# Kernel optimization log

Hardware: AMD Instinct MI355X
Metric: run time of the kernel (lower is better)

## Reference

```python
import jax, jax.numpy as jnp
import numpy as np

N_NODES = 50000
N_EDGES = 800000
D = 64


def setup_inputs() -> dict:
    key = jax.random.key(0)
    ks = jax.random.split(key, 8)
    x = jax.random.normal(ks[0], (N_NODES, D), dtype=jnp.float32)
    edge_index = jax.random.randint(ks[1], (2, N_EDGES), 0, N_NODES, dtype=jnp.int64)
    # GCNConv params (PyG: Linear without bias inside lin, bias added after aggregation)
    def glorot(k, fan_in, fan_out):
        lim = (6.0 / (fan_in + fan_out)) ** 0.5
        return jax.random.uniform(k, (fan_in, fan_out), jnp.float32, -lim, lim)
    W1 = glorot(ks[2], D, D); b1 = jnp.zeros((D,), jnp.float32)
    W2 = glorot(ks[3], D, D); b2 = jnp.zeros((D,), jnp.float32)
    W3 = glorot(ks[4], D, D); b3 = jnp.zeros((D,), jnp.float32)
    return {"x": x, "edge_index": edge_index,
            "W1": W1, "b1": b1, "W2": W2, "b2": b2, "W3": W3, "b3": b3}


def _gcn_norm(edge_index, n_nodes, dtype):
    # Add self-loops, compute symmetric normalization D^-1/2 (A+I) D^-1/2 (PyG GCNConv default).
    loop = jnp.arange(n_nodes, dtype=edge_index.dtype)
    src = jnp.concatenate([edge_index[0], loop])  # message source j
    dst = jnp.concatenate([edge_index[1], loop])  # aggregation target i
    deg = jax.ops.segment_sum(jnp.ones_like(dst, dtype=dtype), dst, num_segments=n_nodes)
    dinv = jnp.where(deg > 0, jax.lax.rsqrt(deg), 0.0)
    norm = dinv[src] * dinv[dst]  # [E + N]
    return src, dst, norm


def _gcn_conv(x, src, dst, norm, W, b, n_nodes):
    h = x @ W                              # [N, D_out]
    msg = h[src] * norm[:, None]           # gather + scale, [E+N, D_out]
    out = jax.ops.segment_sum(msg, dst, num_segments=n_nodes)  # scatter-add
    return out + b


def reference(x, edge_index, W1, b1, W2, b2, W3, b3):
    n = x.shape[0]
    src, dst, norm = _gcn_norm(edge_index, n, x.dtype)
    # layer 0: conv -> relu -> residual
    h = _gcn_conv(x, src, dst, norm, W1, b1, n)
    h = jax.nn.relu(h) + x
    # layer 1: conv -> relu -> residual
    r = h
    h = _gcn_conv(h, src, dst, norm, W2, b2, n)
    h = jax.nn.relu(h) + r
    # layer 2 (final): conv only
    h = _gcn_conv(h, src, dst, norm, W3, b3, n)
    return h
```

## Files before the change

### kernel.cpp

```cpp
#include <hip/hip_runtime.h>
#include <hip/hip_bf16.h>


#define CAP 64
#define EDGE_CHUNK 1024

typedef __attribute__((ext_vector_type(8))) short bf16x8;
typedef __attribute__((ext_vector_type(4))) float f32x4;

__device__ inline unsigned pack_bf16(float a, float b) {
    union { float f; unsigned i; } ua, ub;
    ua.f = a; ub.f = b;
    unsigned x = (ua.i + 0x7fffu + ((ua.i >> 16) & 1u)) >> 16;
    unsigned y = (ub.i + 0x7fffu + ((ub.i >> 16) & 1u)) >> 16;
    return x | (y << 16);
}
__device__ inline unsigned short to_bf16(float a) {
    union { float f; unsigned i; } u; u.f = a;
    return (unsigned short)((u.i + 0x7fffu + ((u.i >> 16) & 1u)) >> 16);
}
__device__ inline void acc_bf16x2(unsigned u, float& a, float& b) {
    union { unsigned i; float f; } lo, hi;
    lo.i = u << 16;
    hi.i = u & 0xffff0000u;
    a += lo.f; b += hi.f;
}

__device__ inline void gather_plane(const unsigned short* __restrict__ gp,
                                    const int* __restrict__ lst, int deg, int off,
                                    float& a0, float& a1, float& a2, float& a3,
                                    float& a4, float& a5, float& a6, float& a7) {
    int nfull = deg >> 3;
    int4 ja, jb;
    if (nfull > 0) { ja = *(const int4*)&lst[0]; jb = *(const int4*)&lst[4]; }
    for (int b = 0; b < nfull; b++) {
        int4 na = ja, nb = jb;
        if (b + 1 < nfull) {
            na = *(const int4*)&lst[(b + 1) * 8];
            nb = *(const int4*)&lst[(b + 1) * 8 + 4];
        }
        uint4 w0 = *(const uint4*)&gp[(size_t)ja.x * 32 + off];
        uint4 w1 = *(const uint4*)&gp[(size_t)ja.y * 32 + off];
        uint4 w2 = *(const uint4*)&gp[(size_t)ja.z * 32 + off];
        uint4 w3 = *(const uint4*)&gp[(size_t)ja.w * 32 + off];
        uint4 w4 = *(const uint4*)&gp[(size_t)jb.x * 32 + off];
        uint4 w5 = *(const uint4*)&gp[(size_t)jb.y * 32 + off];
        uint4 w6 = *(const uint4*)&gp[(size_t)jb.z * 32 + off];
        uint4 w7 = *(const uint4*)&gp[(size_t)jb.w * 32 + off];
        acc_bf16x2(w0.x, a0, a1); acc_bf16x2(w0.y, a2, a3);
        acc_bf16x2(w0.z, a4, a5); acc_bf16x2(w0.w, a6, a7);
        acc_bf16x2(w1.x, a0, a1); acc_bf16x2(w1.y, a2, a3);
        acc_bf16x2(w1.z, a4, a5); acc_bf16x2(w1.w, a6, a7);
        acc_bf16x2(w2.x, a0, a1); acc_bf16x2(w2.y, a2, a3);
        acc_bf16x2(w2.z, a4, a5); acc_bf16x2(w2.w, a6, a7);
        acc_bf16x2(w3.x, a0, a1); acc_bf16x2(w3.y, a2, a3);
        acc_bf16x2(w3.z, a4, a5); acc_bf16x2(w3.w, a6, a7);
        acc_bf16x2(w4.x, a0, a1); acc_bf16x2(w4.y, a2, a3);
        acc_bf16x2(w4.z, a4, a5); acc_bf16x2(w4.w, a6, a7);
        acc_bf16x2(w5.x, a0, a1); acc_bf16x2(w5.y, a2, a3);
        acc_bf16x2(w5.z, a4, a5); acc_bf16x2(w5.w, a6, a7);
        acc_bf16x2(w6.x, a0, a1); acc_bf16x2(w6.y, a2, a3);
        acc_bf16x2(w6.z, a4, a5); acc_bf16x2(w6.w, a6, a7);
        acc_bf16x2(w7.x, a0, a1); acc_bf16x2(w7.y, a2, a3);
        acc_bf16x2(w7.z, a4, a5); acc_bf16x2(w7.w, a6, a7);
        ja = na; jb = nb;
    }
    int k = nfull * 8;
    if (k + 4 <= deg) {
        int4 j4 = *(const int4*)&lst[k];
        uint4 w0 = *(const uint4*)&gp[(size_t)j4.x * 32 + off];
        uint4 w1 = *(const uint4*)&gp[(size_t)j4.y * 32 + off];
        uint4 w2 = *(const uint4*)&gp[(size_t)j4.z * 32 + off];
        uint4 w3 = *(const uint4*)&gp[(size_t)j4.w * 32 + off];
        acc_bf16x2(w0.x, a0, a1); acc_bf16x2(w0.y, a2, a3);
        acc_bf16x2(w0.z, a4, a5); acc_bf16x2(w0.w, a6, a7);
        acc_bf16x2(w1.x, a0, a1); acc_bf16x2(w1.y, a2, a3);
        acc_bf16x2(w1.z, a4, a5); acc_bf16x2(w1.w, a6, a7);
        acc_bf16x2(w2.x, a0, a1); acc_bf16x2(w2.y, a2, a3);
        acc_bf16x2(w2.z, a4, a5); acc_bf16x2(w2.w, a6, a7);
        acc_bf16x2(w3.x, a0, a1); acc_bf16x2(w3.y, a2, a3);
        acc_bf16x2(w3.z, a4, a5); acc_bf16x2(w3.w, a6, a7);
        k += 4;
    }
    for (; k < deg; k++) {
        uint4 v = *(const uint4*)&gp[(size_t)lst[k] * 32 + off];
        acc_bf16x2(v.x, a0, a1); acc_bf16x2(v.y, a2, a3);
        acc_bf16x2(v.z, a4, a5); acc_bf16x2(v.w, a6, a7);
    }
}

__global__ void fill_kernel(const int* __restrict__ src, const int* __restrict__ dst,
                            int* __restrict__ cnt, int* __restrict__ adj,
                            int E, int npc) {
    int cls = blockIdx.x & 7;
    int base = (blockIdx.x >> 3) * EDGE_CHUNK;
    int end = min(base + EDGE_CHUNK, E);
    int lo = cls * npc, hi = lo + npc;
    for (int e = base + threadIdx.x; e < end; e += blockDim.x) {
        int d = dst[e];
        if (d >= lo && d < hi) {
            int p = atomicAdd(&cnt[d], 1);
            adj[(size_t)d * CAP + p] = src[e];
        }
    }
}

__device__ inline void stage_W(const float* __restrict__ W, unsigned short* Wb, int t) {
#pragma unroll
    for (int e0 = 0; e0 < 2; e0++) {
        int e = t + e0 * 256;
        int sc = e >> 6;
        int l  = e & 63;
        int s = sc >> 2, c = sc & 3;
        int nn = c * 16 + (l & 15);
        int kb = s * 32 + (l >> 4) * 8;
        const float* wp = &W[(size_t)kb * 64 + nn];
        unsigned q0 = pack_bf16(wp[0 * 64], wp[1 * 64]);
        unsigned q1 = pack_bf16(wp[2 * 64], wp[3 * 64]);
        unsigned q2 = pack_bf16(wp[4 * 64], wp[5 * 64]);
        unsigned q3 = pack_bf16(wp[6 * 64], wp[7 * 64]);
        *(uint4*)&Wb[e * 8] = make_uint4(q0, q1, q2, q3);
    }
}

__global__ __launch_bounds__(256, 4) void gemm_kernel(const float* __restrict__ in,
                                                      const float* __restrict__ W,
                                                      const int* __restrict__ cnt,
                                                      unsigned short* __restrict__ gLo,
                                                      unsigned short* __restrict__ gHi,
                                                      int n) {
    __shared__ unsigned short Wb[512 * 8];
    int t = threadIdx.x;
    stage_W(W, Wb, t);

    int wv = t >> 6;
    int lane = t & 63;
    int quad = lane >> 4;
    int m16 = lane & 15;

    int rowA = blockIdx.x * 64 + wv * 16 + m16;
    union { bf16x8 v; uint4 u; } a0, a1;
    {
        float4 f0 = make_float4(0, 0, 0, 0), f1 = f0, f2 = f0, f3 = f0;
        if (rowA < n) {
            const float* rp = &in[(size_t)rowA * 64];
            f0 = *(const float4*)&rp[quad * 8];
            f1 = *(const float4*)&rp[quad * 8 + 4];
            f2 = *(const float4*)&rp[32 + quad * 8];
            f3 = *(const float4*)&rp[32 + quad * 8 + 4];
        }
        a0.u = make_uint4(pack_bf16(f0.x, f0.y), pack_bf16(f0.z, f0.w),
                          pack_bf16(f1.x, f1.y), pack_bf16(f1.z, f1.w));
        a1.u = make_uint4(pack_bf16(f2.x, f2.y), pack_bf16(f2.z, f2.w),
                          pack_bf16(f3.x, f3.y), pack_bf16(f3.z, f3.w));
    }
    __syncthreads();

    f32x4 acc[4];
#pragma unroll
    for (int c = 0; c < 4; c++) {
        bf16x8 b0 = *(const bf16x8*)&Wb[((size_t)(0 * 4 + c) * 64 + lane) * 8];
        bf16x8 b1 = *(const bf16x8*)&Wb[((size_t)(1 * 4 + c) * 64 + lane) * 8];
        f32x4 z = {0.f, 0.f, 0.f, 0.f};
        z = __builtin_amdgcn_mfma_f32_16x16x32_bf16(a0.v, b0, z, 0, 0, 0);
        z = __builtin_amdgcn_mfma_f32_16x16x32_bf16(a1.v, b1, z, 0, 0, 0);
        acc[c] = z;
    }

    int lrow = wv * 16 + quad * 4;
    float dv[4];
#pragma unroll
    for (int r = 0; r < 4; r++) {
        int row = blockIdx.x * 64 + lrow + r;
        dv[r] = (row < n) ? rsqrtf((float)(cnt[row] + 1)) : 0.f;
    }
    __syncthreads();
    unsigned short* Ofrag = Wb;
#pragma unroll
    for (int c = 0; c < 4; c++) {
#pragma unroll
        for (int r = 0; r < 4; r++)
            Ofrag[(size_t)(lrow + r) * 64 + c * 16 + m16] = to_bf16(acc[c][r] * dv[r]);
    }
    __syncthreads();
#pragma unroll
    for (int it = 0; it < 2; it++) {
        int unit = t + it * 256;
        int row = unit >> 3, chv = unit & 7;
        int grow = blockIdx.x * 64 + row;
        if (grow < n) {
            unsigned short* op = (chv < 4) ? gLo : gHi;
            *(uint4*)&op[(size_t)grow * 32 + (chv & 3) * 8] =
                *(const uint4*)&Ofrag[(size_t)row * 64 + chv * 8];
        }
    }
}

template <int WRITE_H, int RES_BF16>
__global__ __launch_bounds__(256, 4) void aggemm_kernel(
        const unsigned short* __restrict__ gLo,
        const unsigned short* __restrict__ gHi,
        const int* __restrict__ cnt,
        const int* __restrict__ adj,
        const float* __restrict__ bias,
        const void* __restrict__ res_p,
        const float* __restrict__ W,
        unsigned short* __restrict__ h_out,
        unsigned short* __restrict__ goLo,
        unsigned short* __restrict__ goHi,
        int n) {
    __shared__ unsigned short Wb[512 * 8];
    __shared__ unsigned short Afrag[2048];
    __shared__ float dsh[32];
    int t = threadIdx.x;

    int r  = t >> 3;
    int lg = t & 7;
    const int c8 = lg * 8;
    const int po = (lg & 3) * 8;
    int i = blockIdx.x * 32 + r;
    bool valid = i < n;
    int deg = valid ? cnt[i] : 0;
    const int* lst = adj + (size_t)i * CAP;
    const unsigned short* mp = (lg < 4) ? gLo : gHi;

    float a0 = 0.f, a1 = 0.f, a2 = 0.f, a3 = 0.f;
    float a4 = 0.f, a5 = 0.f, a6 = 0.f, a7 = 0.f;
    float r0 = 0.f, r1 = 0.f, r2 = 0.f, r3 = 0.f;
    float r4 = 0.f, r5 = 0.f, r6 = 0.f, r7 = 0.f;
    if (valid) {
        {
            uint4 v = *(const uint4*)&mp[(size_t)i * 32 + po];
            acc_bf16x2(v.x, a0, a1); acc_bf16x2(v.y, a2, a3);
            acc_bf16x2(v.z, a4, a5); acc_bf16x2(v.w, a6, a7);
        }
        if (RES_BF16) {
            const unsigned short* rp = (const unsigned short*)res_p;
            uint4 rv = *(const uint4*)&rp[(size_t)i * 64 + c8];
            acc_bf16x2(rv.x, r0, r1); acc_bf16x2(rv.y, r2, r3);
            acc_bf16x2(rv.z, r4, r5); acc_bf16x2(rv.w, r6, r7);
        } else {
            const float* rp = (const float*)res_p;
            float4 q0 = *(const float4*)&rp[(size_t)i * 64 + c8];
            float4 q1 = *(const float4*)&rp[(size_t)i * 64 + c8 + 4];
            r0 = q0.x; r1 = q0.y; r2 = q0.z; r3 = q0.w;
            r4 = q1.x; r5 = q1.y; r6 = q1.z; r7 = q1.w;
        }
    }
    if (lg < 4)
        gather_plane(mp, lst, deg, po, a0, a1, a2, a3, a4, a5, a6, a7);
    __syncthreads();
    if (lg >= 4)
        gather_plane(mp, lst, deg, po, a0, a1, a2, a3, a4, a5, a6, a7);

    float dvv = 0.f;
    float v0 = 0.f, v1 = 0.f, v2 = 0.f, v3 = 0.f;
    float v4 = 0.f, v5 = 0.f, v6 = 0.f, v7 = 0.f;
    if (valid) {
        dvv = rsqrtf((float)(deg + 1));
        float4 b0 = *(const float4*)&bias[c8];
        float4 b1 = *(const float4*)&bias[c8 + 4];
        v0 = fmaxf(dvv * a0 + b0.x, 0.f) + r0;
        v1 = fmaxf(dvv * a1 + b0.y, 0.f) + r1;
        v2 = fmaxf(dvv * a2 + b0.z, 0.f) + r2;
        v3 = fmaxf(dvv * a3 + b0.w, 0.f) + r3;
        v4 = fmaxf(dvv * a4 + b1.x, 0.f) + r4;
        v5 = fmaxf(dvv * a5 + b1.y, 0.f) + r5;
        v6 = fmaxf(dvv * a6 + b1.z, 0.f) + r6;
        v7 = fmaxf(dvv * a7 + b1.w, 0.f) + r7;
    }
    uint4 pk;
    pk.x = pack_bf16(v0, v1);
    pk.y = pack_bf16(v2, v3);
    pk.z = pack_bf16(v4, v5);
    pk.w = pack_bf16(v6, v7);
    if (WRITE_H && valid)
        *(uint4*)&h_out[(size_t)i * 64 + c8] = pk;
    stage_W(W, Wb, t);
    {
        int sA = r >> 4, mA = r & 15;
        *(uint4*)&Afrag[((size_t)(sA * 8 + lg) * 16 + mA) * 8] = pk;
        if (lg == 0) dsh[r] = dvv;
    }
    __syncthreads();

    int wv = t >> 6;
    int lane = t & 63;
    int quad = lane >> 4;
    int m16 = lane & 15;
    int sB = wv & 1;
    int ch = wv >> 1;
    bf16x8 af0 = *(const bf16x8*)&Afrag[((size_t)(sB * 8 + quad) * 16 + m16) * 8];
    bf16x8 af1 = *(const bf16x8*)&Afrag[((size_t)(sB * 8 + 4 + quad) * 16 + m16) * 8];
    int lrow = sB * 16 + quad * 4;
    float dv2[4];
#pragma unroll
    for (int rr = 0; rr < 4; rr++)
        dv2[rr] = dsh[lrow + rr];
    __syncthreads();
    f32x4 acc[2];
#pragma unroll
    for (int c2 = 0; c2 < 2; c2++) {
        int c = ch * 2 + c2;
        bf16x8 b0 = *(const bf16x8*)&Wb[((size_t)(0 * 4 + c) * 64 + lane) * 8];
        bf16x8 b1 = *(const bf16x8*)&Wb[((size_t)(1 * 4 + c) * 64 + lane) * 8];
        f32x4 z = {0.f, 0.f, 0.f, 0.f};
        z = __builtin_amdgcn_mfma_f32_16x16x32_bf16(af0, b0, z, 0, 0, 0);
        z = __builtin_amdgcn_mfma_f32_16x16x32_bf16(af1, b1, z, 0, 0, 0);
        acc[c2] = z;
    }
#pragma unroll
    for (int c2 = 0; c2 < 2; c2++) {
        int c = ch * 2 + c2;
#pragma unroll
        for (int rr = 0; rr < 4; rr++)
            Afrag[(size_t)(lrow + rr) * 64 + c * 16 + m16] = to_bf16(acc[c2][rr] * dv2[rr]);
    }
    __syncthreads();
    {
        int orow = blockIdx.x * 32 + r;
        if (orow < n) {
            unsigned short* op = (lg < 4) ? goLo : goHi;
            *(uint4*)&op[(size_t)orow * 32 + po] =
                *(const uint4*)&Afrag[(size_t)r * 64 + c8];
        }
    }
}

__global__ __launch_bounds__(256, 4) void agg_kernel(const unsigned short* __restrict__ gLo,
                                                     const unsigned short* __restrict__ gHi,
                                                     const int* __restrict__ cnt,
                                                     const int* __restrict__ adj,
                                                     const float* __restrict__ bias,
                                                     float* __restrict__ out, int n) {
    int t = threadIdx.x;
    int lg = t & 7;
    int r = t >> 3;
    int i = blockIdx.x * 32 + r;
    bool valid = i < n;
    int deg = valid ? cnt[i] : 0;
    const int* lst = adj + (size_t)i * CAP;
    const int c8 = lg * 8;
    const int po = (lg & 3) * 8;
    const unsigned short* mp = (lg < 4) ? gLo : gHi;
    float a0 = 0.f, a1 = 0.f, a2 = 0.f, a3 = 0.f;
    float a4 = 0.f, a5 = 0.f, a6 = 0.f, a7 = 0.f;
    if (valid) {
        uint4 v = *(const uint4*)&mp[(size_t)i * 32 + po];
        acc_bf16x2(v.x, a0, a1); acc_bf16x2(v.y, a2, a3);
        acc_bf16x2(v.z, a4, a5); acc_bf16x2(v.w, a6, a7);
    }
    if (lg < 4)
        gather_plane(mp, lst, deg, po, a0, a1, a2, a3, a4, a5, a6, a7);
    __syncthreads();
    if (lg >= 4)
        gather_plane(mp, lst, deg, po, a0, a1, a2, a3, a4, a5, a6, a7);
    if (!valid) return;
    float dv = rsqrtf((float)(deg + 1));
    float4 b0 = *(const float4*)&bias[c8];
    float4 b1 = *(const float4*)&bias[c8 + 4];
    float4 o0, o1;
    o0.x = dv * a0 + b0.x; o0.y = dv * a1 + b0.y;
    o0.z = dv * a2 + b0.z; o0.w = dv * a3 + b0.w;
    o1.x = dv * a4 + b1.x; o1.y = dv * a5 + b1.y;
    o1.z = dv * a6 + b1.z; o1.w = dv * a7 + b1.w;
    size_t rowoff = (size_t)i * 64 + c8;
    *(float4*)&out[rowoff] = o0;
    *(float4*)&out[rowoff + 4] = o1;
}

extern "C" void kernel_launch(void* const* d_in, const int* in_sizes, int n_in,
                              void* d_out, int out_size, void* d_ws, size_t ws_size,
                              hipStream_t stream) {
    const float* x  = (const float*)d_in[0];
    const int*   ei = (const int*)d_in[1];
    const float* W1 = (const float*)d_in[2];
    const float* b1 = (const float*)d_in[3];
    const float* W2 = (const float*)d_in[4];
    const float* b2 = (const float*)d_in[5];
    const float* W3 = (const float*)d_in[6];
    const float* b3 = (const float*)d_in[7];
    float* out = (float*)d_out;

    const int N = in_sizes[0] / 64;
    const int E = in_sizes[1] / 2;
    const int* src = ei;
    const int* dst = ei + E;
    const int npc = (N + 7) / 8;
    const int nEdgeChunks = (E + EDGE_CHUNK - 1) / EDGE_CHUNK;

    char* p = (char*)d_ws;
    const int Na = ((N + 63) / 64) * 64;
    int*            cnt  = (int*)p;            p += (size_t)Na * 4;
    int*            adj  = (int*)p;            p += ((size_t)N + 1) * CAP * 4;
    unsigned short* gaLo = (unsigned short*)p; p += (size_t)N * 32 * 2;
    unsigned short* gaHi = (unsigned short*)p; p += (size_t)N * 32 * 2;
    unsigned short* gbLo = (unsigned short*)p; p += (size_t)N * 32 * 2;
    unsigned short* gbHi = (unsigned short*)p; p += (size_t)N * 32 * 2;
    unsigned short* h1   = (unsigned short*)p; p += (size_t)N * 64 * 2;

    const int tileBlocks = (N + 63) / 64;
    const int halfBlocks = (N + 31) / 32;

    hipMemsetAsync(cnt, 0, (size_t)N * 4, stream);
    fill_kernel<<<nEdgeChunks * 8, 256, 0, stream>>>(src, dst, cnt, adj, E, npc);

    gemm_kernel<<<tileBlocks, 256, 0, stream>>>(x, W1, cnt, gaLo, gaHi, N);
    aggemm_kernel<1, 0><<<halfBlocks, 256, 0, stream>>>(gaLo, gaHi, cnt, adj, b1,
                                                        (const void*)x, W2, h1,
                                                        gbLo, gbHi, N);
    aggemm_kernel<0, 1><<<halfBlocks, 256, 0, stream>>>(gbLo, gbHi, cnt, adj, b2,
                                                        (const void*)h1, W3, nullptr,
                                                        gaLo, gaHi, N);
    agg_kernel<<<halfBlocks, 256, 0, stream>>>(gaLo, gaHi, cnt, adj, b3, out, N);
}
```

Measured before the change: 209.9 us.

## Halve aggregation block size: each thread gathers both lo and hi planes serially

Aggregation kernels now use 128 threads per 32 nodes, 4 threads per node. Each thread gathers the low 32-feature plane and then the high plane, where before 8 threads per node each took one plane. Each wave in the fused GEMM now computes all four output column tiles for its 16 rows, and W staging is templated on thread count. This halves thread count and duplicates adjacency index loads per thread. The likely aim is to reuse each neighbor index for both planes and cut launch overhead, at the cost of less parallelism for hiding gather latency and more registers per thread.

```diff
diff --git a/kernel.cpp b/kernel.cpp
--- a/kernel.cpp
+++ b/kernel.cpp
@@ -105,10 +105,11 @@
     }
 }
 
+template <int NT>
 __device__ inline void stage_W(const float* __restrict__ W, unsigned short* Wb, int t) {
 #pragma unroll
-    for (int e0 = 0; e0 < 2; e0++) {
-        int e = t + e0 * 256;
+    for (int e0 = 0; e0 < 512 / NT; e0++) {
+        int e = t + e0 * NT;
         int sc = e >> 6;
         int l  = e & 63;
         int s = sc >> 2, c = sc & 3;
@@ -131,7 +132,7 @@
                                                       int n) {
     __shared__ unsigned short Wb[512 * 8];
     int t = threadIdx.x;
-    stage_W(W, Wb, t);
+    stage_W<256>(W, Wb, t);
 
     int wv = t >> 6;
     int lane = t & 63;
@@ -197,7 +198,7 @@
 }
 
 template <int WRITE_H, int RES_BF16>
-__global__ __launch_bounds__(256, 4) void aggemm_kernel(
+__global__ __launch_bounds__(128, 4) void aggemm_kernel(
         const unsigned short* __restrict__ gLo,
         const unsigned short* __restrict__ gHi,
         const int* __restrict__ cnt,
@@ -214,73 +215,103 @@
     __shared__ float dsh[32];
     int t = threadIdx.x;
 
-    int r  = t >> 3;
-    int lg = t & 7;
-    const int c8 = lg * 8;
-    const int po = (lg & 3) * 8;
+    int r  = t >> 2;
+    int l4 = t & 3;
+    const int po = l4 * 8;
     int i = blockIdx.x * 32 + r;
     bool valid = i < n;
     int deg = valid ? cnt[i] : 0;
     const int* lst = adj + (size_t)i * CAP;
-    const unsigned short* mp = (lg < 4) ? gLo : gHi;
-
-    float a0 = 0.f, a1 = 0.f, a2 = 0.f, a3 = 0.f;
-    float a4 = 0.f, a5 = 0.f, a6 = 0.f, a7 = 0.f;
-    float r0 = 0.f, r1 = 0.f, r2 = 0.f, r3 = 0.f;
-    float r4 = 0.f, r5 = 0.f, r6 = 0.f, r7 = 0.f;
+
+    float la0 = 0.f, la1 = 0.f, la2 = 0.f, la3 = 0.f;
+    float la4 = 0.f, la5 = 0.f, la6 = 0.f, la7 = 0.f;
+    float ha0 = 0.f, ha1 = 0.f, ha2 = 0.f, ha3 = 0.f;
+    float ha4 = 0.f, ha5 = 0.f, ha6 = 0.f, ha7 = 0.f;
+
     if (valid) {
-        {
-            uint4 v = *(const uint4*)&mp[(size_t)i * 32 + po];
-            acc_bf16x2(v.x, a0, a1); acc_bf16x2(v.y, a2, a3);
-            acc_bf16x2(v.z, a4, a5); acc_bf16x2(v.w, a6, a7);
-        }
-        if (RES_BF16) {
-            const unsigned short* rp = (const unsigned short*)res_p;
-            uint4 rv = *(const uint4*)&rp[(size_t)i * 64 + c8];
-            acc_bf16x2(rv.x, r0, r1); acc_bf16x2(rv.y, r2, r3);
-            acc_bf16x2(rv.z, r4, r5); acc_bf16x2(rv.w, r6, r7);
-        } else {
-            const float* rp = (const float*)res_p;
-            float4 q0 = *(const float4*)&rp[(size_t)i * 64 + c8];
-            float4 q1 = *(const float4*)&rp[(size_t)i * 64 + c8 + 4];
-            r0 = q0.x; r1 = q0.y; r2 = q0.z; r3 = q0.w;
-            r4 = q1.x; r5 = q1.y; r6 = q1.z; r7 = q1.w;
-        }
-    }
-    if (lg < 4)
-        gather_plane(mp, lst, deg, po, a0, a1, a2, a3, a4, a5, a6, a7);
-    __syncthreads();
-    if (lg >= 4)
-        gather_plane(mp, lst, deg, po, a0, a1, a2, a3, a4, a5, a6, a7);
+        uint4 v = *(const uint4*)&gLo[(size_t)i * 32 + po];
+        acc_bf16x2(v.x, la0, la1); acc_bf16x2(v.y, la2, la3);
+        acc_bf16x2(v.z, la4, la5); acc_bf16x2(v.w, la6, la7);
+    }
+    gather_plane(gLo, lst, deg, po, la0, la1, la2, la3, la4, la5, la6, la7);
+    __syncthreads();
+    if (valid) {
+        uint4 v = *(const uint4*)&gHi[(size_t)i * 32 + po];
+        acc_bf16x2(v.x, ha0, ha1); acc_bf16x2(v.y, ha2, ha3);
+        acc_bf16x2(v.z, ha4, ha5); acc_bf16x2(v.w, ha6, ha7);
+    }
+    gather_plane(gHi, lst, deg, po, ha0, ha1, ha2, ha3, ha4, ha5, ha6, ha7);
 
     float dvv = 0.f;
-    float v0 = 0.f, v1 = 0.f, v2 = 0.f, v3 = 0.f;
-    float v4 = 0.f, v5 = 0.f, v6 = 0.f, v7 = 0.f;
-    if (valid) {
-        dvv = rsqrtf((float)(deg + 1));
-        float4 b0 = *(const float4*)&bias[c8];
-        float4 b1 = *(const float4*)&bias[c8 + 4];
-        v0 = fmaxf(dvv * a0 + b0.x, 0.f) + r0;
-        v1 = fmaxf(dvv * a1 + b0.y, 0.f) + r1;
-        v2 = fmaxf(dvv * a2 + b0.z, 0.f) + r2;
-        v3 = fmaxf(dvv * a3 + b0.w, 0.f) + r3;
-        v4 = fmaxf(dvv * a4 + b1.x, 0.f) + r4;
-        v5 = fmaxf(dvv * a5 + b1.y, 0.f) + r5;
-        v6 = fmaxf(dvv * a6 + b1.z, 0.f) + r6;
-        v7 = fmaxf(dvv * a7 + b1.w, 0.f) + r7;
-    }
-    uint4 pk;
-    pk.x = pack_bf16(v0, v1);
-    pk.y = pack_bf16(v2, v3);
-    pk.z = pack_bf16(v4, v5);
-    pk.w = pack_bf16(v6, v7);
-    if (WRITE_H && valid)
-        *(uint4*)&h_out[(size_t)i * 64 + c8] = pk;
-    stage_W(W, Wb, t);
+    uint4 pkL, pkH;
+    {
+        float v0 = 0.f, v1 = 0.f, v2 = 0.f, v3 = 0.f;
+        float v4 = 0.f, v5 = 0.f, v6 = 0.f, v7 = 0.f;
+        float w0 = 0.f, w1 = 0.f, w2 = 0.f, w3 = 0.f;
+        float w4 = 0.f, w5 = 0.f, w6 = 0.f, w7 = 0.f;
+        if (valid) {
+            dvv = rsqrtf((float)(deg + 1));
+            float4 bL0 = *(const float4*)&bias[po];
+            float4 bL1 = *(const float4*)&bias[po + 4];
+            float4 bH0 = *(const float4*)&bias[32 + po];
+            float4 bH1 = *(const float4*)&bias[32 + po + 4];
+            float rL[8], rH[8];
+            if (RES_BF16) {
+                const unsigned short* rp = (const unsigned short*)res_p;
+                uint4 rv0 = *(const uint4*)&rp[(size_t)i * 64 + po];
+                uint4 rv1 = *(const uint4*)&rp[(size_t)i * 64 + 32 + po];
+                acc_bf16x2(rv0.x, rL[0] = 0, rL[1] = 0);
+                rL[0] = 0; rL[1] = 0; rL[2] = 0; rL[3] = 0;
+                rL[4] = 0; rL[5] = 0; rL[6] = 0; rL[7] = 0;
+                rH[0] = 0; rH[1] = 0; rH[2] = 0; rH[3] = 0;
+                rH[4] = 0; rH[5] = 0; rH[6] = 0; rH[7] = 0;
+                acc_bf16x2(rv0.x, rL[0], rL[1]); acc_bf16x2(rv0.y, rL[2], rL[3]);
+                acc_bf16x2(rv0.z, rL[4], rL[5]); acc_bf16x2(rv0.w, rL[6], rL[7]);
+                acc_bf16x2(rv1.x, rH[0], rH[1]); acc_bf16x2(rv1.y, rH[2], rH[3]);
+                acc_bf16x2(rv1.z, rH[4], rH[5]); acc_bf16x2(rv1.w, rH[6], rH[7]);
+            } else {
+                const float* rp = (const float*)res_p;
+                float4 q0 = *(const float4*)&rp[(size_t)i * 64 + po];
+                float4 q1 = *(const float4*)&rp[(size_t)i * 64 + po + 4];
+                float4 q2 = *(const float4*)&rp[(size_t)i * 64 + 32 + po];
+                float4 q3 = *(const float4*)&rp[(size_t)i * 64 + 32 + po + 4];
+                rL[0] = q0.x; rL[1] = q0.y; rL[2] = q0.z; rL[3] = q0.w;
+                rL[4] = q1.x; rL[5] = q1.y; rL[6] = q1.z; rL[7] = q1.w;
+                rH[0] = q2.x; rH[1] = q2.y; rH[2] = q2.z; rH[3] = q2.w;
+                rH[4] = q3.x; rH[5] = q3.y; rH[6] = q3.z; rH[7] = q3.w;
+            }
+            v0 = fmaxf(dvv * la0 + bL0.x, 0.f) + rL[0];
+            v1 = fmaxf(dvv * la1 + bL0.y, 0.f) + rL[1];
+            v2 = fmaxf(dvv * la2 + bL0.z, 0.f) + rL[2];
+            v3 = fmaxf(dvv * la3 + bL0.w, 0.f) + rL[3];
+            v4 = fmaxf(dvv * la4 + bL1.x, 0.f) + rL[4];
+            v5 = fmaxf(dvv * la5 + bL1.y, 0.f) + rL[5];
+            v6 = fmaxf(dvv * la6 + bL1.z, 0.f) + rL[6];
+            v7 = fmaxf(dvv * la7 + bL1.w, 0.f) + rL[7];
+            w0 = fmaxf(dvv * ha0 + bH0.x, 0.f) + rH[0];
+            w1 = fmaxf(dvv * ha1 + bH0.y, 0.f) + rH[1];
+            w2 = fmaxf(dvv * ha2 + bH0.z, 0.f) + rH[2];
+            w3 = fmaxf(dvv * ha3 + bH0.w, 0.f) + rH[3];
+            w4 = fmaxf(dvv * ha4 + bH1.x, 0.f) + rH[4];
+            w5 = fmaxf(dvv * ha5 + bH1.y, 0.f) + rH[5];
+            w6 = fmaxf(dvv * ha6 + bH1.z, 0.f) + rH[6];
+            w7 = fmaxf(dvv * ha7 + bH1.w, 0.f) + rH[7];
+        }
+        pkL.x = pack_bf16(v0, v1); pkL.y = pack_bf16(v2, v3);
+        pkL.z = pack_bf16(v4, v5); pkL.w = pack_bf16(v6, v7);
+        pkH.x = pack_bf16(w0, w1); pkH.y = pack_bf16(w2, w3);
+        pkH.z = pack_bf16(w4, w5); pkH.w = pack_bf16(w6, w7);
+    }
+    if (WRITE_H && valid) {
+        *(uint4*)&h_out[(size_t)i * 64 + po]      = pkL;
+        *(uint4*)&h_out[(size_t)i * 64 + 32 + po] = pkH;
+    }
+    stage_W<128>(W, Wb, t);
     {
         int sA = r >> 4, mA = r & 15;
-        *(uint4*)&Afrag[((size_t)(sA * 8 + lg) * 16 + mA) * 8] = pk;
-        if (lg == 0) dsh[r] = dvv;
+        *(uint4*)&Afrag[((size_t)(sA * 8 + l4) * 16 + mA) * 8]     = pkL;
+        *(uint4*)&Afrag[((size_t)(sA * 8 + 4 + l4) * 16 + mA) * 8] = pkH;
+        if (l4 == 0) dsh[r] = dvv;
     }
     __syncthreads();
 
@@ -288,8 +319,7 @@
     int lane = t & 63;
     int quad = lane >> 4;
     int m16 = lane & 15;
-    int sB = wv & 1;
-    int ch = wv >> 1;
+    int sB = wv;
     bf16x8 af0 = *(const bf16x8*)&Afrag[((size_t)(sB * 8 + quad) * 16 + m16) * 8];
     bf16x8 af1 = *(const bf16x8*)&Afrag[((size_t)(sB * 8 + 4 + quad) * 16 + m16) * 8];
     int lrow = sB * 16 + quad * 4;
@@ -298,75 +328,87 @@
     for (int rr = 0; rr < 4; rr++)
         dv2[rr] = dsh[lrow + rr];
     __syncthreads();
-    f32x4 acc[2];
-#pragma unroll
-    for (int c2 = 0; c2 < 2; c2++) {
-        int c = ch * 2 + c2;
+    f32x4 acc[4];
+#pragma unroll
+    for (int c = 0; c < 4; c++) {
         bf16x8 b0 = *(const bf16x8*)&Wb[((size_t)(0 * 4 + c) * 64 + lane) * 8];
         bf16x8 b1 = *(const bf16x8*)&Wb[((size_t)(1 * 4 + c) * 64 + lane) * 8];
         f32x4 z = {0.f, 0.f, 0.f, 0.f};
         z = __builtin_amdgcn_mfma_f32_16x16x32_bf16(af0, b0, z, 0, 0, 0);
         z = __builtin_amdgcn_mfma_f32_16x16x32_bf16(af1, b1, z, 0, 0, 0);
-        acc[c2] = z;
-    }
-#pragma unroll
-    for (int c2 = 0; c2 < 2; c2++) {
-        int c = ch * 2 + c2;
+        acc[c] = z;
+    }
+#pragma unroll
+    for (int c = 0; c < 4; c++) {
 #pragma unroll
         for (int rr = 0; rr < 4; rr++)
-            Afrag[(size_t)(lrow + rr) * 64 + c * 16 + m16] = to_bf16(acc[c2][rr] * dv2[rr]);
-    }
-    __syncthreads();
-    {
-        int orow = blockIdx.x * 32 + r;
+            Afrag[(size_t)(lrow + rr) * 64 + c * 16 + m16] = to_bf16(acc[c][rr] * dv2[rr]);
+    }
+    __syncthreads();
+#pragma unroll
+    for (int it = 0; it < 2; it++) {
+        int unit = t + it * 128;
+        int row = unit >> 3, chv = unit & 7;
+        int orow = blockIdx.x * 32 + row;
         if (orow < n) {
-            unsigned short* op = (lg < 4) ? goLo : goHi;
-            *(uint4*)&op[(size_t)orow * 32 + po] =
-                *(const uint4*)&Afrag[(size_t)r * 64 + c8];
-        }
-    }
-}
-
-__global__ __launch_bounds__(256, 4) void agg_kernel(const unsigned short* __restrict__ gLo,
+            unsigned short* op = (chv < 4) ? goLo : goHi;
+            *(uint4*)&op[(size_t)orow * 32 + (chv & 3) * 8] =
+                *(const uint4*)&Afrag[(size_t)row * 64 + chv * 8];
+        }
+    }
+}
+
+__global__ __launch_bounds__(128, 4) void agg_kernel(const unsigned short* __restrict__ gLo,
                                                      const unsigned short* __restrict__ gHi,
                                                      const int* __restrict__ cnt,
                                                      const int* __restrict__ adj,
                                                      const float* __restrict__ bias,
                                                      float* __restrict__ out, int n) {
     int t = threadIdx.x;
-    int lg = t & 7;
-    int r = t >> 3;
+    int r = t >> 2;
+    int l4 = t & 3;
+    const int po = l4 * 8;
     int i = blockIdx.x * 32 + r;
     bool valid = i < n;
     int deg = valid ? cnt[i] : 0;
     const int* lst = adj + (size_t)i * CAP;
-    const int c8 = lg * 8;
-    const int po = (lg & 3) * 8;
-    const unsigned short* mp = (lg < 4) ? gLo : gHi;
-    float a0 = 0.f, a1 = 0.f, a2 = 0.f, a3 = 0.f;
-    float a4 = 0.f, a5 = 0.f, a6 = 0.f, a7 = 0.f;
+    float la0 = 0.f, la1 = 0.f, la2 = 0.f, la3 = 0.f;
+    float la4 = 0.f, la5 = 0.f, la6 = 0.f, la7 = 0.f;
+    float ha0 = 0.f, ha1 = 0.f, ha2 = 0.f, ha3 = 0.f;
+    float ha4 = 0.f, ha5 = 0.f, ha6 = 0.f, ha7 = 0.f;
     if (valid) {
-        uint4 v = *(const uint4*)&mp[(size_t)i * 32 + po];
-        acc_bf16x2(v.x, a0, a1); acc_bf16x2(v.y, a2, a3);
-        acc_bf16x2(v.z, a4, a5); acc_bf16x2(v.w, a6, a7);
-    }
-    if (lg < 4)
-        gather_plane(mp, lst, deg, po, a0, a1, a2, a3, a4, a5, a6, a7);
-    __syncthreads();
-    if (lg >= 4)
-        gather_plane(mp, lst, deg, po, a0, a1, a2, a3, a4, a5, a6, a7);
+        uint4 v = *(const uint4*)&gLo[(size_t)i * 32 + po];
+        acc_bf16x2(v.x, la0, la1); acc_bf16x2(v.y, la2, la3);
+        acc_bf16x2(v.z, la4, la5); acc_bf16x2(v.w, la6, la7);
+    }
+    gather_plane(gLo, lst, deg, po, la0, la1, la2, la3, la4, la5, la6, la7);
+    __syncthreads();
+    if (valid) {
+        uint4 v = *(const uint4*)&gHi[(size_t)i * 32 + po];
+        acc_bf16x2(v.x, ha0, ha1); acc_bf16x2(v.y, ha2, ha3);
+        acc_bf16x2(v.z, ha4, ha5); acc_bf16x2(v.w, ha6, ha7);
+    }
+    gather_plane(gHi, lst, deg, po, ha0, ha1, ha2, ha3, ha4, ha5, ha6, ha7);
     if (!valid) return;
     float dv = rsqrtf((float)(deg + 1));
-    float4 b0 = *(const float4*)&bias[c8];
-    float4 b1 = *(const float4*)&bias[c8 + 4];
-    float4 o0, o1;
-    o0.x = dv * a0 + b0.x; o0.y = dv * a1 + b0.y;
-    o0.z = dv * a2 + b0.z; o0.w = dv * a3 + b0.w;
-    o1.x = dv * a4 + b1.x; o1.y = dv * a5 + b1.y;
-    o1.z = dv * a6 + b1.z; o1.w = dv * a7 + b1.w;
-    size_t rowoff = (size_t)i * 64 + c8;
-    *(float4*)&out[rowoff] = o0;
-    *(float4*)&out[rowoff + 4] = o1;
+    float4 bL0 = *(const float4*)&bias[po];
+    float4 bL1 = *(const float4*)&bias[po + 4];
+    float4 bH0 = *(const float4*)&bias[32 + po];
+    float4 bH1 = *(const float4*)&bias[32 + po + 4];
+    float4 o0, o1, o2, o3;
+    o0.x = dv * la0 + bL0.x; o0.y = dv * la1 + bL0.y;
+    o0.z = dv * la2 + bL0.z; o0.w = dv * la3 + bL0.w;
+    o1.x = dv * la4 + bL1.x; o1.y = dv * la5 + bL1.y;
+    o1.z = dv * la6 + bL1.z; o1.w = dv * la7 + bL1.w;
+    o2.x = dv * ha0 + bH0.x; o2.y = dv * ha1 + bH0.y;
+    o2.z = dv * ha2 + bH0.z; o2.w = dv * ha3 + bH0.w;
+    o3.x = dv * ha4 + bH1.x; o3.y = dv * ha5 + bH1.y;
+    o3.z = dv * ha6 + bH1.z; o3.w = dv * ha7 + bH1.w;
+    size_t base = (size_t)i * 64;
+    *(float4*)&out[base + po]          = o0;
+    *(float4*)&out[base + po + 4]      = o1;
+    *(float4*)&out[base + 32 + po]     = o2;
+    *(float4*)&out[base + 32 + po + 4] = o3;
 }
 
 extern "C" void kernel_launch(void* const* d_in, const int* in_sizes, int n_in,
@@ -406,11 +448,11 @@
     fill_kernel<<<nEdgeChunks * 8, 256, 0, stream>>>(src, dst, cnt, adj, E, npc);
 
     gemm_kernel<<<tileBlocks, 256, 0, stream>>>(x, W1, cnt, gaLo, gaHi, N);
-    aggemm_kernel<1, 0><<<halfBlocks, 256, 0, stream>>>(gaLo, gaHi, cnt, adj, b1,
+    aggemm_kernel<1, 0><<<halfBlocks, 128, 0, stream>>>(gaLo, gaHi, cnt, adj, b1,
                                                         (const void*)x, W2, h1,
                                                         gbLo, gbHi, N);
-    aggemm_kernel<0, 1><<<halfBlocks, 256, 0, stream>>>(gbLo, gbHi, cnt, adj, b2,
+    aggemm_kernel<0, 1><<<halfBlocks, 128, 0, stream>>>(gbLo, gbHi, cnt, adj, b2,
                                                         (const void*)h1, W3, nullptr,
                                                         gaLo, gaHi, N);
-    agg_kernel<<<halfBlocks, 256, 0, stream>>>(gaLo, gaHi, cnt, adj, b3, out, N);
-}
+    agg_kernel<<<halfBlocks, 128, 0, stream>>>(gaLo, gaHi, cnt, adj, b3, out, N);
+}
```

Result: faster. 186.4 us (-11.2%).
